# Performance work log

Hardware: AMD Instinct MI355X
Metric: run time of the kernel (lower is better)

Reference implementation:

```python
import jax, jax.numpy as jnp
import numpy as np

DIM = 1024

def setup_inputs() -> dict:
    key = jax.random.key(0)
    ks = jax.random.split(key, 6)
    B, T, D = 8, 2048, DIM
    s = 1.0 / np.sqrt(D)
    x = jax.random.normal(ks[0], (B, T, D), dtype=jnp.float32)
    Wq = jax.random.normal(ks[1], (D, D), dtype=jnp.float32) * s
    Wk = jax.random.normal(ks[2], (D, D), dtype=jnp.float32) * s
    Wv = jax.random.normal(ks[3], (D, D), dtype=jnp.float32) * s
    Wp = jax.random.normal(ks[4], (D, D), dtype=jnp.float32) * s
    bp = jax.random.normal(ks[5], (D,), dtype=jnp.float32) * 0.01
    return {"x": x, "Wq": Wq, "Wk": Wk, "Wv": Wv, "Wp": Wp, "bp": bp}

def reference(x, Wq, Wk, Wv, Wp, bp):
    # x: [b, t, d]; weights stored as [d_in, d_out] (torch Linear applies x @ W.T;
    # here we bake the transpose into the stored matrix).
    scale = x.shape[-1] ** (-0.5)
    q = jnp.einsum('btd,de->bte', x, Wq)
    k = jnp.einsum('btd,de->bte', x, Wk)
    v = jnp.einsum('btd,de->bte', x, Wv)
    attn = jax.nn.softmax(jnp.einsum('btd,bTd->btT', q, k) * scale, axis=-1)
    out = jnp.einsum('btT,bTd->btd', attn, v)
    return jnp.einsum('btd,de->bte', out, Wp) + bp
```

## Files before the change

kernel.cpp:

```cpp
#include <hip/hip_runtime.h>


typedef _Float16 half_t;
typedef _Float16 half8 __attribute__((ext_vector_type(8)));
typedef float floatx4 __attribute__((ext_vector_type(4)));

#define GLD16(gp, lp)                                                          \
    __builtin_amdgcn_global_load_lds(                                          \
        (const __attribute__((address_space(1))) void*)(gp),                   \
        (__attribute__((address_space(3))) void*)(lp), 16, 0, 0)

template<int EPI>
__global__ __launch_bounds__(256, 2)
void gemm16(const half_t* __restrict__ A, const half_t* __restrict__ B,
            void* __restrict__ Cv, void* __restrict__ C2, void* __restrict__ C3,
            const float* __restrict__ bias, int K, int lda, int ldb, int ldc,
            long long bsA, long long bsB, long long bsC)
{
    __shared__ half_t As[128 * 32];
    __shared__ half_t Bs[128 * 32];

    const int tid  = threadIdx.x;
    const int lane = tid & 63;
    const int wid  = tid >> 6;
    const int wr   = (wid >> 1) * 64;
    const int wc   = (wid & 1) * 64;
    const long long z = blockIdx.z;
    const int rowBase = blockIdx.y * 128;
    const int colBase = blockIdx.x * 128;

    const int srow = wid * 32 + (lane >> 2);
    const int scol = (lane & 3) * 8;

    const half_t* ga0 = A + z * bsA + (long long)(rowBase + srow) * lda + scol;
    const half_t* ga1 = ga0 + 16LL * lda;
    const half_t* gb0 = B + z * bsB + (long long)(colBase + srow) * ldb + scol;
    const half_t* gb1 = gb0 + 16LL * ldb;
    half_t* la0 = &As[(wid * 32) * 32];
    half_t* la1 = &As[(wid * 32 + 16) * 32];
    half_t* lb0 = &Bs[(wid * 32) * 32];
    half_t* lb1 = &Bs[(wid * 32 + 16) * 32];

    floatx4 acc[4][4];
    #pragma unroll
    for (int m = 0; m < 4; ++m)
        #pragma unroll
        for (int n = 0; n < 4; ++n)
            #pragma unroll
            for (int j = 0; j < 4; ++j) acc[m][n][j] = 0.0f;

    const int fr = lane & 15;
    const int fk = (lane >> 4) * 8;

    for (int kk = 0; kk < K; kk += 32) {
        __syncthreads();
        GLD16(ga0 + kk, la0);
        GLD16(ga1 + kk, la1);
        GLD16(gb0 + kk, lb0);
        GLD16(gb1 + kk, lb1);
        __syncthreads();

        half8 af[4], bf[4];
        #pragma unroll
        for (int m = 0; m < 4; ++m)
            af[m] = *(const half8*)&As[(wr + m * 16 + fr) * 32 + fk];
        #pragma unroll
        for (int n = 0; n < 4; ++n)
            bf[n] = *(const half8*)&Bs[(wc + n * 16 + fr) * 32 + fk];
        #pragma unroll
        for (int m = 0; m < 4; ++m)
            #pragma unroll
            for (int n = 0; n < 4; ++n)
                acc[m][n] = __builtin_amdgcn_mfma_f32_16x16x32_f16(af[m], bf[n], acc[m][n], 0, 0, 0);
    }

    const int ecol = lane & 15;
    const int q4   = (lane >> 4) * 4;
    #pragma unroll
    for (int m = 0; m < 4; ++m) {
        #pragma unroll
        for (int n = 0; n < 4; ++n) {
            const int gcol = colBase + wc + n * 16 + ecol;
            #pragma unroll
            for (int r = 0; r < 4; ++r) {
                const int grow = rowBase + wr + m * 16 + q4 + r;
                float v = acc[m][n][r];
                if (EPI == 0) {
                    ((half_t*)Cv)[z * bsC + (long long)grow * ldc + gcol] = (half_t)v;
                } else if (EPI == 1) {
                    ((float*)Cv)[(long long)grow * ldc + gcol] = v + bias[gcol];
                } else {
                    const int mat = colBase >> 10;
                    const int c   = gcol & 1023;
                    if (mat == 0) {
                        ((half_t*)Cv)[(long long)grow * 1024 + c] = (half_t)(v * 0.03125f);
                    } else if (mat == 1) {
                        ((half_t*)C2)[(long long)grow * 1024 + c] = (half_t)v;
                    } else {
                        const long long bb = grow >> 11;
                        const long long tt = grow & 2047;
                        ((half_t*)C3)[bb * (1024LL * 2048) + (long long)c * 2048 + tt] = (half_t)v;
                    }
                }
            }
        }
    }
}

__global__ __launch_bounds__(256)
void cast16(const float* __restrict__ x, half_t* __restrict__ y)
{
    const long long i = ((long long)blockIdx.x * 256 + threadIdx.x) * 8;
    floatx4 a = *(const floatx4*)(x + i);
    floatx4 b = *(const floatx4*)(x + i + 4);
    half8 h;
    #pragma unroll
    for (int j = 0; j < 4; ++j) { h[j] = (half_t)a[j]; h[j + 4] = (half_t)b[j]; }
    *(half8*)(y + i) = h;
}

__global__ __launch_bounds__(256)
void cast_transpose4(const float* __restrict__ W0, const float* __restrict__ W1,
                     const float* __restrict__ W2, const float* __restrict__ W3,
                     half_t* __restrict__ WT)
{
    const float* W = (blockIdx.z == 0) ? W0 : (blockIdx.z == 1) ? W1
                   : (blockIdx.z == 2) ? W2 : W3;
    half_t* O = WT + (long long)blockIdx.z * 1024 * 1024;
    __shared__ float t[32][33];
    const int bx = blockIdx.x * 32, by = blockIdx.y * 32;
    const int tx = threadIdx.x, ty = threadIdx.y;
    #pragma unroll
    for (int i = 0; i < 32; i += 8)
        t[ty + i][tx] = W[(long long)(by + ty + i) * 1024 + bx + tx];
    __syncthreads();
    #pragma unroll
    for (int i = 0; i < 32; i += 8)
        O[(long long)(bx + ty + i) * 1024 + by + tx] = (half_t)t[tx][ty + i];
}

__global__ __launch_bounds__(256)
void softmax_rows(half_t* __restrict__ S)
{
    const long long base = (long long)blockIdx.x * 2048;
    const int t = threadIdx.x;
    half8 h = *(const half8*)(S + base + t * 8);
    float v[8];
    #pragma unroll
    for (int i = 0; i < 8; ++i) v[i] = (float)h[i];
    float m = -3.0e38f;
    #pragma unroll
    for (int i = 0; i < 8; ++i) m = fmaxf(m, v[i]);
    #pragma unroll
    for (int off = 32; off > 0; off >>= 1) m = fmaxf(m, __shfl_down(m, off));
    __shared__ float redm[4], reds[4];
    const int lane = t & 63, wid = t >> 6;
    if (lane == 0) redm[wid] = m;
    __syncthreads();
    const float M = fmaxf(fmaxf(redm[0], redm[1]), fmaxf(redm[2], redm[3]));
    float s = 0.f;
    #pragma unroll
    for (int i = 0; i < 8; ++i) { v[i] = __expf(v[i] - M); s += v[i]; }
    #pragma unroll
    for (int off = 32; off > 0; off >>= 1) s += __shfl_down(s, off);
    if (lane == 0) reds[wid] = s;
    __syncthreads();
    const float inv = 1.0f / (reds[0] + reds[1] + reds[2] + reds[3]);
    #pragma unroll
    for (int i = 0; i < 8; ++i) h[i] = (half_t)(v[i] * inv);
    *(half8*)(S + base + t * 8) = h;
}

extern "C" void kernel_launch(void* const* d_in, const int* in_sizes, int n_in,
                              void* d_out, int out_size, void* d_ws, size_t ws_size,
                              hipStream_t stream)
{
    const float* x  = (const float*)d_in[0];
    const float* Wq = (const float*)d_in[1];
    const float* Wk = (const float*)d_in[2];
    const float* Wv = (const float*)d_in[3];
    const float* Wp = (const float*)d_in[4];
    const float* bp = (const float*)d_in[5];
    float* out = (float*)d_out;

    char* ws = (char*)d_ws;
    const long long MB = 1024LL * 1024LL;
    half_t* WqkvT = (half_t*)(ws + 0 * MB);
    half_t* WpT   = (half_t*)(ws + 6 * MB);
    half_t* q     = (half_t*)(ws + 8 * MB);
    half_t* k     = (half_t*)(ws + 40 * MB);
    half_t* vT    = (half_t*)(ws + 72 * MB);
    half_t* x16   = (half_t*)(ws + 104 * MB);
    half_t* S     = (half_t*)(ws + 104 * MB);

    dim3 blk(256);
    cast16<<<8192, blk, 0, stream>>>(x, x16);
    cast_transpose4<<<dim3(32, 32, 4), dim3(32, 8), 0, stream>>>(Wq, Wk, Wv, Wp, WqkvT);

    gemm16<2><<<dim3(24, 128, 1), blk, 0, stream>>>(
        x16, WqkvT, q, k, vT, nullptr, 1024, 1024, 1024, 0, 0, 0, 0);

    gemm16<0><<<dim3(16, 16, 8), blk, 0, stream>>>(
        q, k, S, nullptr, nullptr, nullptr, 1024, 1024, 1024, 2048,
        2048LL * 1024, 2048LL * 1024, 2048LL * 2048);

    softmax_rows<<<8 * 2048, blk, 0, stream>>>(S);

    gemm16<0><<<dim3(8, 16, 8), blk, 0, stream>>>(
        S, vT, q, nullptr, nullptr, nullptr, 2048, 2048, 2048, 1024,
        2048LL * 2048, 1024LL * 2048, 2048LL * 1024);

    gemm16<1><<<dim3(8, 128, 1), blk, 0, stream>>>(
        q, WpT, out, nullptr, nullptr, bp, 1024, 1024, 1024, 1024, 0, 0, 0);
}
```

Baseline: 555.0 us.

## Double-buffer LDS tiles in GEMM to overlap global loads with MFMA

The shared-memory tiles become two ping-pong buffers. The next K-slice is issued with global_load_lds before the current slice's MFMAs run, and there is one explicit vmcnt wait plus barrier per iteration instead of two syncthreads. This is meant to hide global-load latency behind compute. LDS use per block doubles to 32KB, which could limit occupancy, and the hand-written waitcnt/barrier ordering has to be correct for the LDS reads.

New measurement: 549.5 us. No clear change (-1.0%).

```diff
diff --git a/kernel.cpp b/kernel.cpp
--- a/kernel.cpp
+++ b/kernel.cpp
@@ -9,6 +9,11 @@
     __builtin_amdgcn_global_load_lds(                                          \
         (const __attribute__((address_space(1))) void*)(gp),                   \
         (__attribute__((address_space(3))) void*)(lp), 16, 0, 0)
+
+#define WAIT_VM0()  asm volatile("s_waitcnt vmcnt(0)" ::: "memory")
+#define BARRIER()   do { asm volatile("" ::: "memory");                        \
+                         __builtin_amdgcn_s_barrier();                         \
+                         asm volatile("" ::: "memory"); } while (0)
 
 template<int EPI>
 __global__ __launch_bounds__(256, 2)
@@ -17,8 +22,8 @@
             const float* __restrict__ bias, int K, int lda, int ldb, int ldc,
             long long bsA, long long bsB, long long bsC)
 {
-    __shared__ half_t As[128 * 32];
-    __shared__ half_t Bs[128 * 32];
+    __shared__ half_t As[2 * 128 * 32];
+    __shared__ half_t Bs[2 * 128 * 32];
 
     const int tid  = threadIdx.x;
     const int lane = tid & 63;
@@ -36,10 +41,8 @@
     const half_t* ga1 = ga0 + 16LL * lda;
     const half_t* gb0 = B + z * bsB + (long long)(colBase + srow) * ldb + scol;
     const half_t* gb1 = gb0 + 16LL * ldb;
-    half_t* la0 = &As[(wid * 32) * 32];
-    half_t* la1 = &As[(wid * 32 + 16) * 32];
-    half_t* lb0 = &Bs[(wid * 32) * 32];
-    half_t* lb1 = &Bs[(wid * 32 + 16) * 32];
+    const int lso0 = (wid * 32) * 32;
+    const int lso1 = (wid * 32 + 16) * 32;
 
     floatx4 acc[4][4];
     #pragma unroll
@@ -51,27 +54,41 @@
 
     const int fr = lane & 15;
     const int fk = (lane >> 4) * 8;
-
-    for (int kk = 0; kk < K; kk += 32) {
-        __syncthreads();
-        GLD16(ga0 + kk, la0);
-        GLD16(ga1 + kk, la1);
-        GLD16(gb0 + kk, lb0);
-        GLD16(gb1 + kk, lb1);
-        __syncthreads();
+    const int nIter = K >> 5;
+
+    GLD16(ga0, &As[lso0]);
+    GLD16(ga1, &As[lso1]);
+    GLD16(gb0, &Bs[lso0]);
+    GLD16(gb1, &Bs[lso1]);
+    WAIT_VM0();
+    BARRIER();
+
+    for (int it = 0; it < nIter; ++it) {
+        const int cur = (it & 1) * 4096;
+        const int nxt = 4096 - cur;
+        if (it + 1 < nIter) {
+            const int kk = (it + 1) << 5;
+            GLD16(ga0 + kk, &As[nxt + lso0]);
+            GLD16(ga1 + kk, &As[nxt + lso1]);
+            GLD16(gb0 + kk, &Bs[nxt + lso0]);
+            GLD16(gb1 + kk, &Bs[nxt + lso1]);
+        }
 
         half8 af[4], bf[4];
         #pragma unroll
         for (int m = 0; m < 4; ++m)
-            af[m] = *(const half8*)&As[(wr + m * 16 + fr) * 32 + fk];
+            af[m] = *(const half8*)&As[cur + (wr + m * 16 + fr) * 32 + fk];
         #pragma unroll
         for (int n = 0; n < 4; ++n)
-            bf[n] = *(const half8*)&Bs[(wc + n * 16 + fr) * 32 + fk];
+            bf[n] = *(const half8*)&Bs[cur + (wc + n * 16 + fr) * 32 + fk];
         #pragma unroll
         for (int m = 0; m < 4; ++m)
             #pragma unroll
             for (int n = 0; n < 4; ++n)
                 acc[m][n] = __builtin_amdgcn_mfma_f32_16x16x32_f16(af[m], bf[n], acc[m][n], 0, 0, 0);
+
+        WAIT_VM0();
+        BARRIER();
     }
 
     const int ecol = lane & 15;
```
